# Optimization experiments

Measured on AMD Instinct MI355X. Metric: run time of the kernel, lower is better.

The kernel has to match this reference:

```python
import jax, jax.numpy as jnp
import numpy as np
from jax import lax

HIDDEN = 2048
VOCAB = 7
MAX_LENGTH = 1024


def setup_inputs() -> dict:
    key = jax.random.key(0)
    ks = jax.random.split(key, 8)
    s = 0.02  # small init scale, mimics trained-weight magnitude
    return {
        "h0": jax.random.normal(ks[0], (1, HIDDEN), jnp.float32),
        "c0": jax.random.normal(ks[1], (1, HIDDEN), jnp.float32),
        "W_ih": jax.random.normal(ks[2], (4 * HIDDEN, VOCAB), jnp.float32) * s,
        "W_hh": jax.random.normal(ks[3], (4 * HIDDEN, HIDDEN), jnp.float32) * s,
        "b_ih": jax.random.normal(ks[4], (4 * HIDDEN,), jnp.float32) * s,
        "b_hh": jax.random.normal(ks[5], (4 * HIDDEN,), jnp.float32) * s,
        "W_out": jax.random.normal(ks[6], (VOCAB, HIDDEN), jnp.float32) * s,
        "b_out": jax.random.normal(ks[7], (VOCAB,), jnp.float32) * s,
    }


def reference(h0, c0, W_ih, W_hh, b_ih, b_hh, W_out, b_out):
    H = h0.shape[-1]
    V = W_out.shape[0]
    # initial decoder input: one-hot at index V-1 (SOS), shape [1, V]
    x0 = jnp.zeros((1, V), h0.dtype).at[0, V - 1].set(1.0)

    def step(carry, _):
        x, h, c = carry
        xr = jax.nn.relu(x)
        # PyTorch LSTM: gates = x W_ih^T + b_ih + h W_hh^T + b_hh, order i,f,g,o
        gates = xr @ W_ih.T + b_ih + h @ W_hh.T + b_hh  # [1, 4H]
        i, f, g, o = jnp.split(gates, 4, axis=-1)
        c2 = jax.nn.sigmoid(f) * c + jax.nn.sigmoid(i) * jnp.tanh(g)
        h2 = jax.nn.sigmoid(o) * jnp.tanh(c2)
        logits = h2 @ W_out.T + b_out  # [1, V]
        # greedy feedback: one-hot of argmax (topk(1) equivalent)
        nxt = jax.nn.one_hot(jnp.argmax(logits, axis=-1), V, dtype=h0.dtype)
        return (nxt, h2, c2), logits[0]

    (_, hN, cN), outs = lax.scan(step, (x0, h0, c0), None, length=MAX_LENGTH)
    log_probs = jax.nn.log_softmax(outs, axis=-1)  # [MAX_LENGTH, V]
    return log_probs, hN, cN
```

## Files before the change

kernel.cpp:

```cpp
#include <hip/hip_runtime.h>
#include <hip/hip_cooperative_groups.h>

namespace cg = cooperative_groups;

#define HIDDEN   2048
#define VOCAB    7
#define STEPS    1024
#define NBLOCKS  512
#define NTHREADS 256
#define NWAVES   (NTHREADS / 64)
#define FAN      8
#define NLEAF    (NBLOCKS / FAN)

typedef unsigned long long u64;

__device__ __align__(256) float g_h[3][HIDDEN];
__device__ __align__(256) float g_p0[NLEAF][64];
__device__ __align__(256) float g_p1[NLEAF * 8];
__device__ __align__(256) int   g_c0[NLEAF * 32];
__device__ __align__(256) int   g_c2[32];
__device__ __align__(256) u64   g_pub[8 * 16];
__device__ float g_c[HIDDEN];
__device__ float g_partfb[NBLOCKS * VOCAB];
__device__ int   g_xi;

__device__ __forceinline__ float sigm(float x) { return 1.0f / (1.0f + expf(-x)); }

#define LOAD_AG(p)     __hip_atomic_load((p), __ATOMIC_RELAXED, __HIP_MEMORY_SCOPE_AGENT)
#define STORE_AG(p, v) __hip_atomic_store((p), (v), __ATOMIC_RELAXED, __HIP_MEMORY_SCOPE_AGENT)
#define RMW_ADD_AG(p)  __hip_atomic_fetch_add((p), 1, __ATOMIC_RELAXED, __HIP_MEMORY_SCOPE_AGENT)
#define VM_DRAIN()     asm volatile("s_waitcnt vmcnt(0)" ::: "memory")
#define C_FENCE()      asm volatile("" ::: "memory")

__device__ __forceinline__ float4 h_pair(const u64* h8, int m) {
    u64 lo = LOAD_AG((u64*)&h8[2 * m]);
    u64 hi = LOAD_AG((u64*)&h8[2 * m + 1]);
    float4 r;
    r.x = __uint_as_float((unsigned)lo);
    r.y = __uint_as_float((unsigned)(lo >> 32));
    r.z = __uint_as_float((unsigned)hi);
    r.w = __uint_as_float((unsigned)(hi >> 32));
    return r;
}

__device__ __forceinline__ float sel7(const float w[VOCAB], int xi) {
    float r = w[0];
    #pragma unroll
    for (int v = 1; v < VOCAB; ++v) r = (xi == v) ? w[v] : r;
    return r;
}

__device__ __forceinline__ float slot_reduce(float x) {
    x += __shfl_down(x, 28, 64);
    x += __shfl_down(x, 14, 64);
    x += __shfl_down(x, 7, 64);
    return x;
}

__global__ __launch_bounds__(NTHREADS, 2)
void coop_kernel(const float* __restrict__ h0,  const float* __restrict__ c0,
                 const float* __restrict__ W_ih, const float* __restrict__ W_hh,
                 const float* __restrict__ b_ih, const float* __restrict__ b_hh,
                 const float* __restrict__ W_out, const float* __restrict__ b_out,
                 float* __restrict__ out)
{
    cg::grid_group grid = cg::this_grid();
    const int tid  = threadIdx.x;
    const int gid  = blockIdx.x * NTHREADS + tid;
    const int lane = tid & 63;
    const int wib  = tid >> 6;
    const int j    = blockIdx.x * NWAVES + wib;

    const int leaf  = blockIdx.x >> 3;
    const int slot0 = blockIdx.x & 7;
    const int rep   = blockIdx.x >> 6;

    __shared__ float s_part[NWAVES][VOCAB];
    __shared__ u64   s_gx;

    if (gid < HIDDEN) STORE_AG(&g_h[0][gid], h0[gid]);
    if (blockIdx.x == 0) {
        if (tid < NLEAF) STORE_AG(&g_c0[tid * 32], 0);
        if (tid == 0)    STORE_AG(&g_c2[0], 0);
        if (tid < 8)     STORE_AG(&g_pub[tid * 16], (u64)0);
    }

    const float4* Wr0 = (const float4*)(W_hh + (size_t)j * HIDDEN);
    const float4* Wr1 = (const float4*)(W_hh + (size_t)(j + HIDDEN) * HIDDEN);
    const float4* Wr2 = (const float4*)(W_hh + (size_t)(j + 2 * HIDDEN) * HIDDEN);
    const float4* Wr3 = (const float4*)(W_hh + (size_t)(j + 3 * HIDDEN) * HIDDEN);

    float bsum0 = 0.f, bsum1 = 0.f, bsum2 = 0.f, bsum3 = 0.f;
    float cv = 0.f, h_fin = 0.f;
    float wih0[VOCAB], wih1[VOCAB], wih2[VOCAB], wih3[VOCAB];
    if (lane == 0) {
        bsum0 = b_ih[j]              + b_hh[j];
        bsum1 = b_ih[j + HIDDEN]     + b_hh[j + HIDDEN];
        bsum2 = b_ih[j + 2 * HIDDEN] + b_hh[j + 2 * HIDDEN];
        bsum3 = b_ih[j + 3 * HIDDEN] + b_hh[j + 3 * HIDDEN];
        cv = c0[j];
        #pragma unroll
        for (int v = 0; v < VOCAB; ++v) {
            wih0[v] = W_ih[(size_t)j * VOCAB + v];
            wih1[v] = W_ih[(size_t)(j + HIDDEN) * VOCAB + v];
            wih2[v] = W_ih[(size_t)(j + 2 * HIDDEN) * VOCAB + v];
            wih3[v] = W_ih[(size_t)(j + 3 * HIDDEN) * VOCAB + v];
        }
    }
    const float wout = (lane < VOCAB) ? W_out[lane * HIDDEN + j] : 0.0f;
    float bov[VOCAB];
    #pragma unroll
    for (int v = 0; v < VOCAB; ++v) bov[v] = b_out[v];

    grid.sync();

    int xi = VOCAB - 1;
    int rb = 0, wbuf = 1;

    for (int t = 0; t < STEPS; ++t) {
        const u64* h8 = (const u64*)g_h[rb];

        float4 hreg[8];
        #pragma unroll
        for (int it = 0; it < 8; ++it) hreg[it] = h_pair(h8, it * 64 + lane);

        float a0 = 0.f, a1 = 0.f, a2 = 0.f, a3 = 0.f;
        #pragma unroll
        for (int it = 0; it < 8; ++it) {
            const float4 hv = hreg[it];
            const float4 w0 = Wr0[it * 64 + lane];
            const float4 w1 = Wr1[it * 64 + lane];
            const float4 w2 = Wr2[it * 64 + lane];
            const float4 w3 = Wr3[it * 64 + lane];
            a0 += w0.x * hv.x + w0.y * hv.y + w0.z * hv.z + w0.w * hv.w;
            a1 += w1.x * hv.x + w1.y * hv.y + w1.z * hv.z + w1.w * hv.w;
            a2 += w2.x * hv.x + w2.y * hv.y + w2.z * hv.z + w2.w * hv.w;
            a3 += w3.x * hv.x + w3.y * hv.y + w3.z * hv.z + w3.w * hv.w;
        }
        #pragma unroll
        for (int off = 32; off > 0; off >>= 1) {
            a0 += __shfl_down(a0, off, 64);
            a1 += __shfl_down(a1, off, 64);
            a2 += __shfl_down(a2, off, 64);
            a3 += __shfl_down(a3, off, 64);
        }

        float h2v = 0.0f;
        if (lane == 0) {
            const float gi = a0 + bsum0 + sel7(wih0, xi);
            const float gf = a1 + bsum1 + sel7(wih1, xi);
            const float gg = a2 + bsum2 + sel7(wih2, xi);
            const float go = a3 + bsum3 + sel7(wih3, xi);
            cv  = sigm(gf) * cv + sigm(gi) * tanhf(gg);
            h2v = sigm(go) * tanhf(cv);
            h_fin = h2v;
            STORE_AG(&g_h[wbuf][j], h2v);
        }
        h2v = __shfl(h2v, 0, 64);

        if (lane < VOCAB) s_part[wib][lane] = h2v * wout;
        __syncthreads();

        if (wib == 0) {
            if (lane < VOCAB)
                STORE_AG(&g_p0[leaf][slot0 * VOCAB + lane],
                         s_part[0][lane] + s_part[1][lane] + s_part[2][lane] + s_part[3][lane]);
            VM_DRAIN();
            int old0 = 0;
            if (lane == 0) old0 = RMW_ADD_AG(&g_c0[leaf * 32]);
            old0 = __shfl(old0, 0, 64);
            C_FENCE();
            if (old0 == (t + 1) * FAN - 1) {
                float x = (lane < FAN * VOCAB) ? LOAD_AG(&g_p0[leaf][lane]) : 0.0f;
                x = slot_reduce(x);
                if (lane < VOCAB) STORE_AG(&g_p1[leaf * 8 + lane], x);
                VM_DRAIN();
                int old2 = 0;
                if (lane == 0) old2 = RMW_ADD_AG(&g_c2[0]);
                old2 = __shfl(old2, 0, 64);
                C_FENCE();
                if (old2 == (t + 1) * NLEAF - 1) {
                    float l[VOCAB];
                    #pragma unroll
                    for (int v = 0; v < VOCAB; ++v) {
                        float s = LOAD_AG(&g_p1[lane * 8 + v]);
                        #pragma unroll
                        for (int off = 32; off > 0; off >>= 1) s += __shfl_down(s, off, 64);
                        l[v] = s;
                    }
                    if (lane == 0) {
                        float mx = -1e30f;
                        #pragma unroll
                        for (int v = 0; v < VOCAB; ++v) { l[v] += bov[v]; mx = fmaxf(mx, l[v]); }
                        float se = 0.0f;
                        #pragma unroll
                        for (int v = 0; v < VOCAB; ++v) se += expf(l[v] - mx);
                        const float lse = mx + logf(se);
                        int am = 0; float best = l[0];
                        #pragma unroll
                        for (int v = 1; v < VOCAB; ++v) if (l[v] > best) { best = l[v]; am = v; }
                        #pragma unroll
                        for (int v = 0; v < VOCAB; ++v) out[t * VOCAB + v] = l[v] - lse;
                        const u64 val = ((u64)(unsigned)(t + 1) << 32) | (u64)(unsigned)am;
                        #pragma unroll
                        for (int r = 0; r < 8; ++r) STORE_AG(&g_pub[r * 16], val);
                    }
                }
            }
        }

        if (tid == 0) {
            u64 cur = LOAD_AG(&g_pub[rep * 16]);
            while ((unsigned)(cur >> 32) != (unsigned)(t + 1)) {
                __builtin_amdgcn_s_sleep(1);
                cur = LOAD_AG(&g_pub[rep * 16]);
            }
            s_gx = cur;
        }
        C_FENCE();
        __syncthreads();
        xi = (int)(unsigned)s_gx;

        rb = wbuf;
        wbuf = (wbuf + 1 == 3) ? 0 : wbuf + 1;
    }

    if (lane == 0) {
        out[STEPS * VOCAB + j]          = h_fin;
        out[STEPS * VOCAB + HIDDEN + j] = cv;
    }
}

__global__ __launch_bounds__(NTHREADS)
void fb_init(const float* __restrict__ h0, const float* __restrict__ c0) {
    int gid = blockIdx.x * NTHREADS + threadIdx.x;
    if (gid < HIDDEN) { g_h[0][gid] = h0[gid]; g_c[gid] = c0[gid]; }
    if (gid == 0) g_xi = VOCAB - 1;
}

__global__ __launch_bounds__(NTHREADS, 2)
void fb_step(const float* __restrict__ W_ih, const float* __restrict__ W_hh,
             const float* __restrict__ b_ih, const float* __restrict__ b_hh,
             const float* __restrict__ W_out, int t)
{
    const int tid  = threadIdx.x;
    const int lane = tid & 63;
    const int wib  = tid >> 6;
    const int j    = blockIdx.x * NWAVES + wib;

    __shared__ float s_part[NWAVES][VOCAB];

    const float4* h4 = (const float4*)g_h[t & 1];
    const float4* Wr0 = (const float4*)(W_hh + (size_t)j * HIDDEN);
    const float4* Wr1 = (const float4*)(W_hh + (size_t)(j + HIDDEN) * HIDDEN);
    const float4* Wr2 = (const float4*)(W_hh + (size_t)(j + 2 * HIDDEN) * HIDDEN);
    const float4* Wr3 = (const float4*)(W_hh + (size_t)(j + 3 * HIDDEN) * HIDDEN);

    float a0 = 0.f, a1 = 0.f, a2 = 0.f, a3 = 0.f;
    #pragma unroll
    for (int it = 0; it < 8; ++it) {
        const float4 hv = h4[it * 64 + lane];
        const float4 w0 = Wr0[it * 64 + lane];
        const float4 w1 = Wr1[it * 64 + lane];
        const float4 w2 = Wr2[it * 64 + lane];
        const float4 w3 = Wr3[it * 64 + lane];
        a0 += w0.x * hv.x + w0.y * hv.y + w0.z * hv.z + w0.w * hv.w;
        a1 += w1.x * hv.x + w1.y * hv.y + w1.z * hv.z + w1.w * hv.w;
        a2 += w2.x * hv.x + w2.y * hv.y + w2.z * hv.z + w2.w * hv.w;
        a3 += w3.x * hv.x + w3.y * hv.y + w3.z * hv.z + w3.w * hv.w;
    }
    #pragma unroll
    for (int off = 32; off > 0; off >>= 1) {
        a0 += __shfl_down(a0, off, 64);
        a1 += __shfl_down(a1, off, 64);
        a2 += __shfl_down(a2, off, 64);
        a3 += __shfl_down(a3, off, 64);
    }

    float h2v = 0.0f;
    if (lane == 0) {
        const int xi = g_xi;
        const float gi = a0 + b_ih[j] + b_hh[j] + W_ih[j * VOCAB + xi];
        const float gf = a1 + b_ih[j + HIDDEN] + b_hh[j + HIDDEN] + W_ih[(j + HIDDEN) * VOCAB + xi];
        const float gg = a2 + b_ih[j + 2 * HIDDEN] + b_hh[j + 2 * HIDDEN] + W_ih[(j + 2 * HIDDEN) * VOCAB + xi];
        const float go = a3 + b_ih[j + 3 * HIDDEN] + b_hh[j + 3 * HIDDEN] + W_ih[(j + 3 * HIDDEN) * VOCAB + xi];
        const float cv = sigm(gf) * g_c[j] + sigm(gi) * tanhf(gg);
        h2v = sigm(go) * tanhf(cv);
        g_c[j] = cv;
        g_h[(t + 1) & 1][j] = h2v;
    }
    h2v = __shfl(h2v, 0, 64);

    const float wout = (lane < VOCAB) ? W_out[lane * HIDDEN + j] : 0.0f;
    if (lane < VOCAB) s_part[wib][lane] = h2v * wout;
    __syncthreads();
    if (tid < VOCAB)
        g_partfb[blockIdx.x * VOCAB + tid] =
            s_part[0][tid] + s_part[1][tid] + s_part[2][tid] + s_part[3][tid];
}

__global__ void fb_logits(const float* __restrict__ b_out, float* __restrict__ out, int t) {
    const int lane = threadIdx.x;
    float lg[VOCAB];
    #pragma unroll
    for (int v = 0; v < VOCAB; ++v) {
        float s = 0.0f;
        for (int i = lane; i < NBLOCKS; i += 64) s += g_partfb[i * VOCAB + v];
        #pragma unroll
        for (int off = 32; off > 0; off >>= 1) s += __shfl_down(s, off, 64);
        lg[v] = s;
    }
    if (lane == 0) {
        float l[VOCAB];
        float mx = -1e30f;
        #pragma unroll
        for (int v = 0; v < VOCAB; ++v) { l[v] = lg[v] + b_out[v]; mx = fmaxf(mx, l[v]); }
        float se = 0.0f;
        #pragma unroll
        for (int v = 0; v < VOCAB; ++v) se += expf(l[v] - mx);
        const float lse = mx + logf(se);
        int am = 0; float best = l[0];
        #pragma unroll
        for (int v = 1; v < VOCAB; ++v) if (l[v] > best) { best = l[v]; am = v; }
        #pragma unroll
        for (int v = 0; v < VOCAB; ++v) out[t * VOCAB + v] = l[v] - lse;
        g_xi = am;
    }
}

__global__ __launch_bounds__(NTHREADS)
void fb_fin(float* __restrict__ out) {
    int gid = blockIdx.x * NTHREADS + threadIdx.x;
    if (gid < HIDDEN) {
        out[STEPS * VOCAB + gid]          = g_h[0][gid];
        out[STEPS * VOCAB + HIDDEN + gid] = g_c[gid];
    }
}

extern "C" void kernel_launch(void* const* d_in, const int* in_sizes, int n_in,
                              void* d_out, int out_size, void* d_ws, size_t ws_size,
                              hipStream_t stream)
{
    const float* h0    = (const float*)d_in[0];
    const float* c0    = (const float*)d_in[1];
    const float* W_ih  = (const float*)d_in[2];
    const float* W_hh  = (const float*)d_in[3];
    const float* b_ih  = (const float*)d_in[4];
    const float* b_hh  = (const float*)d_in[5];
    const float* W_out = (const float*)d_in[6];
    const float* b_out = (const float*)d_in[7];
    float* out = (float*)d_out;

    void* args[] = { &h0, &c0, &W_ih, &W_hh, &b_ih, &b_hh, &W_out, &b_out, &out };
    hipError_t e = hipLaunchCooperativeKernel((void*)coop_kernel,
                                              dim3(NBLOCKS), dim3(NTHREADS), args, 0, stream);
    if (e != hipSuccess) {
        fb_init<<<HIDDEN / NTHREADS, NTHREADS, 0, stream>>>(h0, c0);
        for (int t = 0; t < STEPS; ++t) {
            fb_step<<<NBLOCKS, NTHREADS, 0, stream>>>(W_ih, W_hh, b_ih, b_hh, W_out, t);
            fb_logits<<<1, 64, 0, stream>>>(b_out, out, t);
        }
        fb_fin<<<HIDDEN / NTHREADS, NTHREADS, 0, stream>>>(out);
    }
}
```

Baseline: 7.018 ms.

## Move logits to a dedicated block and overlap xi wait with W_hh matvec

Restructures the persistent cooperative kernel: 256 worker blocks of 8 waves compute gate matvecs, and one extra block computes the output logits, log-softmax and argmax from the published h. Workers wait only on an h-generation counter, start the W_hh·h matvec, and fetch the previous token index afterwards, so the argmax latency overlaps the big matvec. The logits partial-sum tree across blocks is replaced by a single-block full dot product. This adds a serial dependency on one block and more spin-polling, and it needs 257 blocks of 512 threads to be co-resident.

```diff
diff --git a/kernel.cpp b/kernel.cpp
--- a/kernel.cpp
+++ b/kernel.cpp
@@ -6,22 +6,22 @@
 #define HIDDEN   2048
 #define VOCAB    7
 #define STEPS    1024
-#define NBLOCKS  512
-#define NTHREADS 256
-#define NWAVES   (NTHREADS / 64)
-#define FAN      8
-#define NLEAF    (NBLOCKS / FAN)
+#define NWB      256
+#define NTHREADS 512
+#define WPB      8
+#define LFAN     16
+#define NLEAF    (NWB / LFAN)
+#define NBLOCKS  (NWB + 1)
 
 typedef unsigned long long u64;
 
 __device__ __align__(256) float g_h[3][HIDDEN];
-__device__ __align__(256) float g_p0[NLEAF][64];
-__device__ __align__(256) float g_p1[NLEAF * 8];
 __device__ __align__(256) int   g_c0[NLEAF * 32];
 __device__ __align__(256) int   g_c2[32];
-__device__ __align__(256) u64   g_pub[8 * 16];
+__device__ __align__(256) int   g_hgen[8 * 32];
+__device__ __align__(256) u64   g_xip[8 * 16];
 __device__ float g_c[HIDDEN];
-__device__ float g_partfb[NBLOCKS * VOCAB];
+__device__ float g_partfb[512 * VOCAB];
 __device__ int   g_xi;
 
 __device__ __forceinline__ float sigm(float x) { return 1.0f / (1.0f + expf(-x)); }
@@ -50,13 +50,6 @@
     return r;
 }
 
-__device__ __forceinline__ float slot_reduce(float x) {
-    x += __shfl_down(x, 28, 64);
-    x += __shfl_down(x, 14, 64);
-    x += __shfl_down(x, 7, 64);
-    return x;
-}
-
 __global__ __launch_bounds__(NTHREADS, 2)
 void coop_kernel(const float* __restrict__ h0,  const float* __restrict__ c0,
                  const float* __restrict__ W_ih, const float* __restrict__ W_hh,
@@ -66,179 +59,180 @@
 {
     cg::grid_group grid = cg::this_grid();
     const int tid  = threadIdx.x;
-    const int gid  = blockIdx.x * NTHREADS + tid;
+    const int bx   = blockIdx.x;
+    const int gid  = bx * NTHREADS + tid;
     const int lane = tid & 63;
     const int wib  = tid >> 6;
-    const int j    = blockIdx.x * NWAVES + wib;
-
-    const int leaf  = blockIdx.x >> 3;
-    const int slot0 = blockIdx.x & 7;
-    const int rep   = blockIdx.x >> 6;
-
-    __shared__ float s_part[NWAVES][VOCAB];
-    __shared__ u64   s_gx;
+
+    __shared__ float s_lg[2][8];
 
     if (gid < HIDDEN) STORE_AG(&g_h[0][gid], h0[gid]);
-    if (blockIdx.x == 0) {
+    if (bx == 0) {
         if (tid < NLEAF) STORE_AG(&g_c0[tid * 32], 0);
         if (tid == 0)    STORE_AG(&g_c2[0], 0);
-        if (tid < 8)     STORE_AG(&g_pub[tid * 16], (u64)0);
-    }
-
-    const float4* Wr0 = (const float4*)(W_hh + (size_t)j * HIDDEN);
-    const float4* Wr1 = (const float4*)(W_hh + (size_t)(j + HIDDEN) * HIDDEN);
-    const float4* Wr2 = (const float4*)(W_hh + (size_t)(j + 2 * HIDDEN) * HIDDEN);
-    const float4* Wr3 = (const float4*)(W_hh + (size_t)(j + 3 * HIDDEN) * HIDDEN);
-
-    float bsum0 = 0.f, bsum1 = 0.f, bsum2 = 0.f, bsum3 = 0.f;
-    float cv = 0.f, h_fin = 0.f;
-    float wih0[VOCAB], wih1[VOCAB], wih2[VOCAB], wih3[VOCAB];
-    if (lane == 0) {
-        bsum0 = b_ih[j]              + b_hh[j];
-        bsum1 = b_ih[j + HIDDEN]     + b_hh[j + HIDDEN];
-        bsum2 = b_ih[j + 2 * HIDDEN] + b_hh[j + 2 * HIDDEN];
-        bsum3 = b_ih[j + 3 * HIDDEN] + b_hh[j + 3 * HIDDEN];
-        cv = c0[j];
-        #pragma unroll
-        for (int v = 0; v < VOCAB; ++v) {
-            wih0[v] = W_ih[(size_t)j * VOCAB + v];
-            wih1[v] = W_ih[(size_t)(j + HIDDEN) * VOCAB + v];
-            wih2[v] = W_ih[(size_t)(j + 2 * HIDDEN) * VOCAB + v];
-            wih3[v] = W_ih[(size_t)(j + 3 * HIDDEN) * VOCAB + v];
-        }
-    }
-    const float wout = (lane < VOCAB) ? W_out[lane * HIDDEN + j] : 0.0f;
-    float bov[VOCAB];
-    #pragma unroll
-    for (int v = 0; v < VOCAB; ++v) bov[v] = b_out[v];
+        if (tid < 8)     { STORE_AG(&g_hgen[tid * 32], 0); STORE_AG(&g_xip[tid * 16], (u64)0); }
+    }
 
     grid.sync();
 
-    int xi = VOCAB - 1;
-    int rb = 0, wbuf = 1;
-
-    for (int t = 0; t < STEPS; ++t) {
-        const u64* h8 = (const u64*)g_h[rb];
-
-        float4 hreg[8];
-        #pragma unroll
-        for (int it = 0; it < 8; ++it) hreg[it] = h_pair(h8, it * 64 + lane);
-
-        float a0 = 0.f, a1 = 0.f, a2 = 0.f, a3 = 0.f;
-        #pragma unroll
-        for (int it = 0; it < 8; ++it) {
-            const float4 hv = hreg[it];
-            const float4 w0 = Wr0[it * 64 + lane];
-            const float4 w1 = Wr1[it * 64 + lane];
-            const float4 w2 = Wr2[it * 64 + lane];
-            const float4 w3 = Wr3[it * 64 + lane];
-            a0 += w0.x * hv.x + w0.y * hv.y + w0.z * hv.z + w0.w * hv.w;
-            a1 += w1.x * hv.x + w1.y * hv.y + w1.z * hv.z + w1.w * hv.w;
-            a2 += w2.x * hv.x + w2.y * hv.y + w2.z * hv.z + w2.w * hv.w;
-            a3 += w3.x * hv.x + w3.y * hv.y + w3.z * hv.z + w3.w * hv.w;
-        }
-        #pragma unroll
-        for (int off = 32; off > 0; off >>= 1) {
-            a0 += __shfl_down(a0, off, 64);
-            a1 += __shfl_down(a1, off, 64);
-            a2 += __shfl_down(a2, off, 64);
-            a3 += __shfl_down(a3, off, 64);
-        }
-
-        float h2v = 0.0f;
+    if (bx < NWB) {
+        const int j    = bx * WPB + wib;
+        const int leaf = bx >> 4;
+        const int rep  = bx >> 5;
+
+        const float4* Wr0 = (const float4*)(W_hh + (size_t)j * HIDDEN);
+        const float4* Wr1 = (const float4*)(W_hh + (size_t)(j + HIDDEN) * HIDDEN);
+        const float4* Wr2 = (const float4*)(W_hh + (size_t)(j + 2 * HIDDEN) * HIDDEN);
+        const float4* Wr3 = (const float4*)(W_hh + (size_t)(j + 3 * HIDDEN) * HIDDEN);
+
+        float bsum0 = 0.f, bsum1 = 0.f, bsum2 = 0.f, bsum3 = 0.f;
+        float cv = 0.f, h_fin = 0.f;
+        float wih0[VOCAB], wih1[VOCAB], wih2[VOCAB], wih3[VOCAB];
         if (lane == 0) {
-            const float gi = a0 + bsum0 + sel7(wih0, xi);
-            const float gf = a1 + bsum1 + sel7(wih1, xi);
-            const float gg = a2 + bsum2 + sel7(wih2, xi);
-            const float go = a3 + bsum3 + sel7(wih3, xi);
-            cv  = sigm(gf) * cv + sigm(gi) * tanhf(gg);
-            h2v = sigm(go) * tanhf(cv);
-            h_fin = h2v;
-            STORE_AG(&g_h[wbuf][j], h2v);
-        }
-        h2v = __shfl(h2v, 0, 64);
-
-        if (lane < VOCAB) s_part[wib][lane] = h2v * wout;
-        __syncthreads();
-
-        if (wib == 0) {
-            if (lane < VOCAB)
-                STORE_AG(&g_p0[leaf][slot0 * VOCAB + lane],
-                         s_part[0][lane] + s_part[1][lane] + s_part[2][lane] + s_part[3][lane]);
+            bsum0 = b_ih[j]              + b_hh[j];
+            bsum1 = b_ih[j + HIDDEN]     + b_hh[j + HIDDEN];
+            bsum2 = b_ih[j + 2 * HIDDEN] + b_hh[j + 2 * HIDDEN];
+            bsum3 = b_ih[j + 3 * HIDDEN] + b_hh[j + 3 * HIDDEN];
+            cv = c0[j];
+            #pragma unroll
+            for (int v = 0; v < VOCAB; ++v) {
+                wih0[v] = W_ih[(size_t)j * VOCAB + v];
+                wih1[v] = W_ih[(size_t)(j + HIDDEN) * VOCAB + v];
+                wih2[v] = W_ih[(size_t)(j + 2 * HIDDEN) * VOCAB + v];
+                wih3[v] = W_ih[(size_t)(j + 3 * HIDDEN) * VOCAB + v];
+            }
+        }
+
+        int rb = 0, wbuf = 1;
+
+        for (int t = 0; t < STEPS; ++t) {
+            int cur = LOAD_AG(&g_hgen[rep * 32]);
+            while (cur < t) { __builtin_amdgcn_s_sleep(2); cur = LOAD_AG(&g_hgen[rep * 32]); }
+            C_FENCE();
+
+            const u64* h8 = (const u64*)g_h[rb];
+            float4 hreg[8];
+            #pragma unroll
+            for (int it = 0; it < 8; ++it) hreg[it] = h_pair(h8, it * 64 + lane);
+
+            float a0 = 0.f, a1 = 0.f, a2 = 0.f, a3 = 0.f;
+            #pragma unroll
+            for (int it = 0; it < 8; ++it) {
+                const float4 hv = hreg[it];
+                const float4 w0 = Wr0[it * 64 + lane];
+                const float4 w1 = Wr1[it * 64 + lane];
+                const float4 w2 = Wr2[it * 64 + lane];
+                const float4 w3 = Wr3[it * 64 + lane];
+                a0 += w0.x * hv.x + w0.y * hv.y + w0.z * hv.z + w0.w * hv.w;
+                a1 += w1.x * hv.x + w1.y * hv.y + w1.z * hv.z + w1.w * hv.w;
+                a2 += w2.x * hv.x + w2.y * hv.y + w2.z * hv.z + w2.w * hv.w;
+                a3 += w3.x * hv.x + w3.y * hv.y + w3.z * hv.z + w3.w * hv.w;
+            }
+            #pragma unroll
+            for (int off = 32; off > 0; off >>= 1) {
+                a0 += __shfl_down(a0, off, 64);
+                a1 += __shfl_down(a1, off, 64);
+                a2 += __shfl_down(a2, off, 64);
+                a3 += __shfl_down(a3, off, 64);
+            }
+
+            int xi = VOCAB - 1;
+            if (t > 0) {
+                u64 px = LOAD_AG(&g_xip[rep * 16]);
+                while ((int)(px >> 32) < t) { __builtin_amdgcn_s_sleep(1); px = LOAD_AG(&g_xip[rep * 16]); }
+                xi = (int)(unsigned)px;
+            }
+            C_FENCE();
+
+            if (lane == 0) {
+                const float gi = a0 + bsum0 + sel7(wih0, xi);
+                const float gf = a1 + bsum1 + sel7(wih1, xi);
+                const float gg = a2 + bsum2 + sel7(wih2, xi);
+                const float go = a3 + bsum3 + sel7(wih3, xi);
+                cv  = sigm(gf) * cv + sigm(gi) * tanhf(gg);
+                const float h2v = sigm(go) * tanhf(cv);
+                h_fin = h2v;
+                STORE_AG(&g_h[wbuf][j], h2v);
+            }
             VM_DRAIN();
-            int old0 = 0;
-            if (lane == 0) old0 = RMW_ADD_AG(&g_c0[leaf * 32]);
-            old0 = __shfl(old0, 0, 64);
-            C_FENCE();
-            if (old0 == (t + 1) * FAN - 1) {
-                float x = (lane < FAN * VOCAB) ? LOAD_AG(&g_p0[leaf][lane]) : 0.0f;
-                x = slot_reduce(x);
-                if (lane < VOCAB) STORE_AG(&g_p1[leaf * 8 + lane], x);
-                VM_DRAIN();
-                int old2 = 0;
-                if (lane == 0) old2 = RMW_ADD_AG(&g_c2[0]);
-                old2 = __shfl(old2, 0, 64);
-                C_FENCE();
-                if (old2 == (t + 1) * NLEAF - 1) {
-                    float l[VOCAB];
-                    #pragma unroll
-                    for (int v = 0; v < VOCAB; ++v) {
-                        float s = LOAD_AG(&g_p1[lane * 8 + v]);
+            __syncthreads();
+
+            if (tid == 0) {
+                const int o0 = RMW_ADD_AG(&g_c0[leaf * 32]);
+                if (o0 == (t + 1) * LFAN - 1) {
+                    const int o2 = RMW_ADD_AG(&g_c2[0]);
+                    if (o2 == (t + 1) * NLEAF - 1) {
                         #pragma unroll
-                        for (int off = 32; off > 0; off >>= 1) s += __shfl_down(s, off, 64);
-                        l[v] = s;
-                    }
-                    if (lane == 0) {
-                        float mx = -1e30f;
-                        #pragma unroll
-                        for (int v = 0; v < VOCAB; ++v) { l[v] += bov[v]; mx = fmaxf(mx, l[v]); }
-                        float se = 0.0f;
-                        #pragma unroll
-                        for (int v = 0; v < VOCAB; ++v) se += expf(l[v] - mx);
-                        const float lse = mx + logf(se);
-                        int am = 0; float best = l[0];
-                        #pragma unroll
-                        for (int v = 1; v < VOCAB; ++v) if (l[v] > best) { best = l[v]; am = v; }
-                        #pragma unroll
-                        for (int v = 0; v < VOCAB; ++v) out[t * VOCAB + v] = l[v] - lse;
-                        const u64 val = ((u64)(unsigned)(t + 1) << 32) | (u64)(unsigned)am;
-                        #pragma unroll
-                        for (int r = 0; r < 8; ++r) STORE_AG(&g_pub[r * 16], val);
+                        for (int r = 0; r < 8; ++r) STORE_AG(&g_hgen[r * 32], t + 1);
                     }
                 }
             }
-        }
-
-        if (tid == 0) {
-            u64 cur = LOAD_AG(&g_pub[rep * 16]);
-            while ((unsigned)(cur >> 32) != (unsigned)(t + 1)) {
-                __builtin_amdgcn_s_sleep(1);
-                cur = LOAD_AG(&g_pub[rep * 16]);
-            }
-            s_gx = cur;
-        }
-        C_FENCE();
-        __syncthreads();
-        xi = (int)(unsigned)s_gx;
-
-        rb = wbuf;
-        wbuf = (wbuf + 1 == 3) ? 0 : wbuf + 1;
-    }
-
-    if (lane == 0) {
-        out[STEPS * VOCAB + j]          = h_fin;
-        out[STEPS * VOCAB + HIDDEN + j] = cv;
-    }
-}
-
-__global__ __launch_bounds__(NTHREADS)
+
+            rb = wbuf;
+            wbuf = (wbuf + 1 == 3) ? 0 : wbuf + 1;
+        }
+
+        if (lane == 0) {
+            out[STEPS * VOCAB + j]          = h_fin;
+            out[STEPS * VOCAB + HIDDEN + j] = cv;
+        }
+    } else {
+        const int v = wib;
+        float bov[VOCAB];
+        #pragma unroll
+        for (int q = 0; q < VOCAB; ++q) bov[q] = b_out[q];
+        const float4* Wo = (const float4*)(W_out + (size_t)(v < VOCAB ? v : 0) * HIDDEN);
+
+        for (int s = 1; s <= STEPS; ++s) {
+            int cur = LOAD_AG(&g_hgen[7 * 32]);
+            while (cur < s) { __builtin_amdgcn_s_sleep(1); cur = LOAD_AG(&g_hgen[7 * 32]); }
+            C_FENCE();
+
+            if (v < VOCAB) {
+                const u64* h8 = (const u64*)g_h[s % 3];
+                float acc = 0.f;
+                #pragma unroll
+                for (int it = 0; it < 8; ++it) {
+                    const float4 hv = h_pair(h8, it * 64 + lane);
+                    const float4 w  = Wo[it * 64 + lane];
+                    acc += w.x * hv.x + w.y * hv.y + w.z * hv.z + w.w * hv.w;
+                }
+                #pragma unroll
+                for (int off = 32; off > 0; off >>= 1) acc += __shfl_down(acc, off, 64);
+                if (lane == 0) s_lg[s & 1][v] = acc;
+            }
+            __syncthreads();
+
+            if (tid == 0) {
+                float l[VOCAB];
+                float mx = -1e30f;
+                #pragma unroll
+                for (int q = 0; q < VOCAB; ++q) { l[q] = s_lg[s & 1][q] + bov[q]; mx = fmaxf(mx, l[q]); }
+                float se = 0.0f;
+                #pragma unroll
+                for (int q = 0; q < VOCAB; ++q) se += expf(l[q] - mx);
+                const float lse = mx + logf(se);
+                int am = 0; float best = l[0];
+                #pragma unroll
+                for (int q = 1; q < VOCAB; ++q) if (l[q] > best) { best = l[q]; am = q; }
+                #pragma unroll
+                for (int q = 0; q < VOCAB; ++q) out[(s - 1) * VOCAB + q] = l[q] - lse;
+                const u64 val = ((u64)(unsigned)s << 32) | (u64)(unsigned)am;
+                #pragma unroll
+                for (int r = 0; r < 8; ++r) STORE_AG(&g_xip[r * 16], val);
+            }
+        }
+    }
+}
+
+__global__ __launch_bounds__(256)
 void fb_init(const float* __restrict__ h0, const float* __restrict__ c0) {
-    int gid = blockIdx.x * NTHREADS + threadIdx.x;
+    int gid = blockIdx.x * 256 + threadIdx.x;
     if (gid < HIDDEN) { g_h[0][gid] = h0[gid]; g_c[gid] = c0[gid]; }
     if (gid == 0) g_xi = VOCAB - 1;
 }
 
-__global__ __launch_bounds__(NTHREADS, 2)
+__global__ __launch_bounds__(256, 2)
 void fb_step(const float* __restrict__ W_ih, const float* __restrict__ W_hh,
              const float* __restrict__ b_ih, const float* __restrict__ b_hh,
              const float* __restrict__ W_out, int t)
@@ -246,9 +240,9 @@
     const int tid  = threadIdx.x;
     const int lane = tid & 63;
     const int wib  = tid >> 6;
-    const int j    = blockIdx.x * NWAVES + wib;
-
-    __shared__ float s_part[NWAVES][VOCAB];
+    const int j    = blockIdx.x * 4 + wib;
+
+    __shared__ float s_part[4][VOCAB];
 
     const float4* h4 = (const float4*)g_h[t & 1];
     const float4* Wr0 = (const float4*)(W_hh + (size_t)j * HIDDEN);
@@ -305,7 +299,7 @@
     #pragma unroll
     for (int v = 0; v < VOCAB; ++v) {
         float s = 0.0f;
-        for (int i = lane; i < NBLOCKS; i += 64) s += g_partfb[i * VOCAB + v];
+        for (int i = lane; i < 512; i += 64) s += g_partfb[i * VOCAB + v];
         #pragma unroll
         for (int off = 32; off > 0; off >>= 1) s += __shfl_down(s, off, 64);
         lg[v] = s;
@@ -328,9 +322,9 @@
     }
 }
 
-__global__ __launch_bounds__(NTHREADS)
+__global__ __launch_bounds__(256)
 void fb_fin(float* __restrict__ out) {
-    int gid = blockIdx.x * NTHREADS + threadIdx.x;
+    int gid = blockIdx.x * 256 + threadIdx.x;
     if (gid < HIDDEN) {
         out[STEPS * VOCAB + gid]          = g_h[0][gid];
         out[STEPS * VOCAB + HIDDEN + gid] = g_c[gid];
@@ -355,11 +349,11 @@
     hipError_t e = hipLaunchCooperativeKernel((void*)coop_kernel,
                                               dim3(NBLOCKS), dim3(NTHREADS), args, 0, stream);
     if (e != hipSuccess) {
-        fb_init<<<HIDDEN / NTHREADS, NTHREADS, 0, stream>>>(h0, c0);
+        fb_init<<<HIDDEN / 256, 256, 0, stream>>>(h0, c0);
         for (int t = 0; t < STEPS; ++t) {
-            fb_step<<<NBLOCKS, NTHREADS, 0, stream>>>(W_ih, W_hh, b_ih, b_hh, W_out, t);
+            fb_step<<<512, 256, 0, stream>>>(W_ih, W_hh, b_ih, b_hh, W_out, t);
             fb_logits<<<1, 64, 0, stream>>>(b_out, out, t);
         }
-        fb_fin<<<HIDDEN / NTHREADS, NTHREADS, 0, stream>>>(out);
-    }
-}
+        fb_fin<<<HIDDEN / 256, 256, 0, stream>>>(out);
+    }
+}
```

Measured after the change: 16.85 ms. 2.4x slower.

## Split per-step sync into h-ready and argmax flags to overlap matvec with logits reduction

Applied to the files above, without the earlier changes.

Per-step synchronisation is split into two flags. An h-generation flag is published as soon as every block has finished its partials, so the next step's W_hh·h matvec can start. The argmax token flag is waited on only after the matvec, right before it is needed for the input-gate term. The two-level partial reduction also becomes one level: the final block sums all 512 per-block partials from a transposed buffer. The intent is to hide the logits reduction and argmax broadcast behind the next step's dot products, at the cost of an extra spin-wait and a wider final reduction.

```diff
diff --git a/kernel.cpp b/kernel.cpp
--- a/kernel.cpp
+++ b/kernel.cpp
@@ -15,11 +15,11 @@
 typedef unsigned long long u64;
 
 __device__ __align__(256) float g_h[3][HIDDEN];
-__device__ __align__(256) float g_p0[NLEAF][64];
-__device__ __align__(256) float g_p1[NLEAF * 8];
+__device__ __align__(256) float g_pt[VOCAB][NBLOCKS];
 __device__ __align__(256) int   g_c0[NLEAF * 32];
 __device__ __align__(256) int   g_c2[32];
-__device__ __align__(256) u64   g_pub[8 * 16];
+__device__ __align__(256) int   g_hgen[8 * 32];
+__device__ __align__(256) u64   g_xip[8 * 16];
 __device__ float g_c[HIDDEN];
 __device__ float g_partfb[NBLOCKS * VOCAB];
 __device__ int   g_xi;
@@ -50,13 +50,6 @@
     return r;
 }
 
-__device__ __forceinline__ float slot_reduce(float x) {
-    x += __shfl_down(x, 28, 64);
-    x += __shfl_down(x, 14, 64);
-    x += __shfl_down(x, 7, 64);
-    return x;
-}
-
 __global__ __launch_bounds__(NTHREADS, 2)
 void coop_kernel(const float* __restrict__ h0,  const float* __restrict__ c0,
                  const float* __restrict__ W_ih, const float* __restrict__ W_hh,
@@ -66,23 +59,23 @@
 {
     cg::grid_group grid = cg::this_grid();
     const int tid  = threadIdx.x;
-    const int gid  = blockIdx.x * NTHREADS + tid;
+    const int bx   = blockIdx.x;
+    const int gid  = bx * NTHREADS + tid;
     const int lane = tid & 63;
     const int wib  = tid >> 6;
-    const int j    = blockIdx.x * NWAVES + wib;
-
-    const int leaf  = blockIdx.x >> 3;
-    const int slot0 = blockIdx.x & 7;
-    const int rep   = blockIdx.x >> 6;
+    const int j    = bx * NWAVES + wib;
+
+    const int leaf = bx >> 3;
+    const int rep  = bx >> 6;
 
     __shared__ float s_part[NWAVES][VOCAB];
-    __shared__ u64   s_gx;
+    __shared__ int   s_xi;
 
     if (gid < HIDDEN) STORE_AG(&g_h[0][gid], h0[gid]);
-    if (blockIdx.x == 0) {
+    if (bx == 0) {
         if (tid < NLEAF) STORE_AG(&g_c0[tid * 32], 0);
         if (tid == 0)    STORE_AG(&g_c2[0], 0);
-        if (tid < 8)     STORE_AG(&g_pub[tid * 16], (u64)0);
+        if (tid < 8)     { STORE_AG(&g_hgen[tid * 32], 0); STORE_AG(&g_xip[tid * 16], (u64)0); }
     }
 
     const float4* Wr0 = (const float4*)(W_hh + (size_t)j * HIDDEN);
@@ -114,12 +107,17 @@
 
     grid.sync();
 
-    int xi = VOCAB - 1;
     int rb = 0, wbuf = 1;
 
     for (int t = 0; t < STEPS; ++t) {
+        if (tid == 0) {
+            int cur = LOAD_AG(&g_hgen[rep * 32]);
+            while (cur < t) { __builtin_amdgcn_s_sleep(2); cur = LOAD_AG(&g_hgen[rep * 32]); }
+        }
+        C_FENCE();
+        __syncthreads();
+
         const u64* h8 = (const u64*)g_h[rb];
-
         float4 hreg[8];
         #pragma unroll
         for (int it = 0; it < 8; ++it) hreg[it] = h_pair(h8, it * 64 + lane);
@@ -145,6 +143,22 @@
             a3 += __shfl_down(a3, off, 64);
         }
 
+        if (tid == 0) {
+            int xi = VOCAB - 1;
+            if (t > 0) {
+                u64 px = LOAD_AG(&g_xip[rep * 16]);
+                while ((int)(unsigned)(px >> 32) < t) {
+                    __builtin_amdgcn_s_sleep(1);
+                    px = LOAD_AG(&g_xip[rep * 16]);
+                }
+                xi = (int)(unsigned)px;
+            }
+            s_xi = xi;
+        }
+        C_FENCE();
+        __syncthreads();
+        const int xi = s_xi;
+
         float h2v = 0.0f;
         if (lane == 0) {
             const float gi = a0 + bsum0 + sel7(wih0, xi);
@@ -163,27 +177,27 @@
 
         if (wib == 0) {
             if (lane < VOCAB)
-                STORE_AG(&g_p0[leaf][slot0 * VOCAB + lane],
+                STORE_AG(&g_pt[lane][bx],
                          s_part[0][lane] + s_part[1][lane] + s_part[2][lane] + s_part[3][lane]);
             VM_DRAIN();
-            int old0 = 0;
-            if (lane == 0) old0 = RMW_ADD_AG(&g_c0[leaf * 32]);
-            old0 = __shfl(old0, 0, 64);
+            int o0 = 0;
+            if (lane == 0) o0 = RMW_ADD_AG(&g_c0[leaf * 32]);
+            o0 = __shfl(o0, 0, 64);
             C_FENCE();
-            if (old0 == (t + 1) * FAN - 1) {
-                float x = (lane < FAN * VOCAB) ? LOAD_AG(&g_p0[leaf][lane]) : 0.0f;
-                x = slot_reduce(x);
-                if (lane < VOCAB) STORE_AG(&g_p1[leaf * 8 + lane], x);
-                VM_DRAIN();
-                int old2 = 0;
-                if (lane == 0) old2 = RMW_ADD_AG(&g_c2[0]);
-                old2 = __shfl(old2, 0, 64);
+            if (o0 == (t + 1) * FAN - 1) {
+                int o2 = 0;
+                if (lane == 0) o2 = RMW_ADD_AG(&g_c2[0]);
+                o2 = __shfl(o2, 0, 64);
                 C_FENCE();
-                if (old2 == (t + 1) * NLEAF - 1) {
+                if (o2 == (t + 1) * NLEAF - 1) {
+                    if (lane < 8) STORE_AG(&g_hgen[lane * 32], t + 1);
                     float l[VOCAB];
                     #pragma unroll
                     for (int v = 0; v < VOCAB; ++v) {
-                        float s = LOAD_AG(&g_p1[lane * 8 + v]);
+                        float s = 0.0f;
+                        #pragma unroll
+                        for (int k = 0; k < NBLOCKS / 64; ++k)
+                            s += LOAD_AG(&g_pt[v][k * 64 + lane]);
                         #pragma unroll
                         for (int off = 32; off > 0; off >>= 1) s += __shfl_down(s, off, 64);
                         l[v] = s;
@@ -203,23 +217,11 @@
                         for (int v = 0; v < VOCAB; ++v) out[t * VOCAB + v] = l[v] - lse;
                         const u64 val = ((u64)(unsigned)(t + 1) << 32) | (u64)(unsigned)am;
                         #pragma unroll
-                        for (int r = 0; r < 8; ++r) STORE_AG(&g_pub[r * 16], val);
+                        for (int r = 0; r < 8; ++r) STORE_AG(&g_xip[r * 16], val);
                     }
                 }
             }
         }
-
-        if (tid == 0) {
-            u64 cur = LOAD_AG(&g_pub[rep * 16]);
-            while ((unsigned)(cur >> 32) != (unsigned)(t + 1)) {
-                __builtin_amdgcn_s_sleep(1);
-                cur = LOAD_AG(&g_pub[rep * 16]);
-            }
-            s_gx = cur;
-        }
-        C_FENCE();
-        __syncthreads();
-        xi = (int)(unsigned)s_gx;
 
         rb = wbuf;
         wbuf = (wbuf + 1 == 3) ? 0 : wbuf + 1;
```

New measurement: 13.55 ms. 93.1% more time.
